# Performance work log

Hardware: AMD Instinct MI355X
Metric: run time of the kernel (lower is better)

Reference implementation:

```python
import jax, jax.numpy as jnp
import numpy as np

QMIN, QMAX = 0.0, 255.0  # uint8 affine quantization range


def setup_inputs() -> dict:
    key = jax.random.key(0)
    ks = jax.random.split(key, 7)
    B, S, IN, OUT = 4, 2048, 4096, 4096
    x = jax.random.normal(ks[0], (B, S, IN), dtype=jnp.float32)
    weight_q = jax.random.randint(ks[1], (OUT, IN), 0, 255, dtype=jnp.int32)
    weight_scales = jax.random.uniform(ks[2], (OUT,), dtype=jnp.float32) * 0.01 + 1e-4
    weight_zero_points = jax.random.randint(ks[3], (OUT,), 0, 255, dtype=jnp.int32)
    act_scales = jax.random.uniform(ks[4], (1,), dtype=jnp.float32) * 0.05 + 1e-3
    act_zero_points = jnp.full((1,), 128, dtype=jnp.int32)
    bias = jax.random.normal(ks[5], (OUT,), dtype=jnp.float32)
    return {
        "x": x,
        "weight_q": weight_q,
        "weight_scales": weight_scales,
        "weight_zero_points": weight_zero_points,
        "act_scales": act_scales,
        "act_zero_points": act_zero_points,
        "bias": bias,
    }


def reference(x, weight_q, weight_scales, weight_zero_points, act_scales, act_zero_points, bias):
    # quantize_from_qparams on activations (per-tensor affine, uint8 range)
    a_zp = act_zero_points.astype(jnp.float32)
    x_q = jnp.clip(jnp.round(x / act_scales) + a_zp, QMIN, QMAX)
    # linear_on_quantized_data: dequantize both operands, fused matmul + bias
    x_deq = (x_q - a_zp) * act_scales  # [B, S, IN]
    w_deq = (weight_q.astype(jnp.float32) - weight_zero_points.astype(jnp.float32)[:, None]) \
            * weight_scales[:, None]  # [OUT, IN], per-output-channel scale/zp
    out = jnp.einsum("bsi,oi->bso", x_deq, w_deq) + bias  # [B, S, OUT]
    return out
```

## Files before the change

### kernel.cpp

```cpp
#include <hip/hip_runtime.h>
#include <hip/hip_bf16.h>

using int32x4 = __attribute__((ext_vector_type(4))) int;

#define BM 256
#define BN 256
#define BKB 128

#define GATE(n) asm volatile("s_waitcnt vmcnt(" #n ")" ::: "memory")

__device__ __forceinline__ void load_lds16(const void* g, void* l) {
    __builtin_amdgcn_global_load_lds(
        (const __attribute__((address_space(1))) unsigned int*)g,
        (__attribute__((address_space(3))) unsigned int*)l, 16, 0, 0);
}

__global__ __launch_bounds__(256) void prep(
    const float* __restrict__ x, const float* __restrict__ act_scale,
    const int* __restrict__ act_zp, char* __restrict__ xs,
    int* __restrict__ rowsum, int K, int M,
    const int4* __restrict__ wq, char4* __restrict__ wsq, long n4)
{
    if (blockIdx.x < (unsigned)M) {
        __shared__ int wsum[4];
        const int row = blockIdx.x;
        const float s = act_scale[0];
        const int zp = act_zp[0];
        const float4* __restrict__ xr = (const float4*)(x + (size_t)row * K);
        char4* __restrict__ xo = (char4*)(xs + (size_t)row * K);
        const int nv = K >> 2;
        int sum = 0;
        for (int i = threadIdx.x; i < nv; i += 256) {
            float4 v = xr[i];
            int q0 = min(max((int)rintf(v.x / s) + zp, 0), 255) - zp;
            int q1 = min(max((int)rintf(v.y / s) + zp, 0), 255) - zp;
            int q2 = min(max((int)rintf(v.z / s) + zp, 0), 255) - zp;
            int q3 = min(max((int)rintf(v.w / s) + zp, 0), 255) - zp;
            sum += q0 + q1 + q2 + q3;
            char4 c;
            c.x = (char)q0; c.y = (char)q1; c.z = (char)q2; c.w = (char)q3;
            xo[i] = c;
        }
        for (int off = 32; off > 0; off >>= 1) sum += __shfl_down(sum, off, 64);
        if ((threadIdx.x & 63) == 0) wsum[threadIdx.x >> 6] = sum;
        __syncthreads();
        if (threadIdx.x == 0) rowsum[row] = wsum[0] + wsum[1] + wsum[2] + wsum[3];
    } else {
        long i = (long)(blockIdx.x - M) * 256 + threadIdx.x;
        if (i >= n4) return;
        int4 v = wq[i];
        char4 c;
        c.x = (char)(v.x - 128); c.y = (char)(v.y - 128);
        c.z = (char)(v.z - 128); c.w = (char)(v.w - 128);
        wsq[i] = c;
    }
}

__global__ __launch_bounds__(512, 2) void gemm_i8(
    const char* __restrict__ Aq, const char* __restrict__ Bq,
    const int* __restrict__ rowsum, const float* __restrict__ wscale,
    const int* __restrict__ wzp, const float* __restrict__ ascale,
    const float* __restrict__ bias, float* __restrict__ C,
    int M, int N, int K)
{
    __shared__ __align__(16) char As[2][BM * BKB];
    __shared__ __align__(16) char Bs[2][BN * BKB];

    const int tid = threadIdx.x;
    const int w   = tid >> 6;
    const int l   = tid & 63;

    const int nwg = gridDim.x;
    const int nbx = N / BN;
    const int orig = blockIdx.x;
    const int xcd = orig & 7;
    const int rest = orig >> 3;
    const int qq = nwg >> 3, rr = nwg & 7;
    const int wg = (xcd < rr ? xcd * (qq + 1) : rr * (qq + 1) + (xcd - rr) * qq)
                   + rest;
    const int n0 = (wg % nbx) * BN;
    const int m0 = (wg / nbx) * BM;

    const int wm = (w & 1) * 128;
    const int wn = (w >> 1) * 64;

    const int lr8 = l >> 3;
    const int csw = (((l & 7) ^ (lr8 & 7)) << 4);
    const int rB0 = w * 16;
    const int rA2 = (w < 4) ? (w * 16) : (128 + (w - 4) * 16);

    const char* sB0 = Bq + (size_t)(n0 + rB0 + lr8) * K + csw;
    const char* sB1 = sB0 + (size_t)128 * K;
    const char* sA2 = Aq + (size_t)(m0 + rA2 + lr8) * K + csw;
    const char* sA3 = sA2 + (size_t)64 * K;
    const size_t k8 = (size_t)8 * K;

    const int oB0 = rB0 * BKB;
    const int oB1 = oB0 + 128 * BKB;
    const int oA2 = rA2 * BKB;
    const int oA3 = oA2 + 64 * BKB;

    const int r   = l & 15;
    const int qk  = l >> 4;
    const int rx  = r & 7;
    const int rof = r * BKB;
    const int ck0 = ((qk ^ rx) << 4);
    const int ck1 = (((4 + qk) ^ rx) << 4);

    int32x4 acc[8][4] = {};
    const int NT = K / BKB;

    load_lds16(sB0,      Bs[0] + oB0);
    load_lds16(sB0 + k8, Bs[0] + oB0 + 1024);
    load_lds16(sB1,      Bs[0] + oB1);
    load_lds16(sB1 + k8, Bs[0] + oB1 + 1024);
    load_lds16(sA2,      As[0] + oA2);
    load_lds16(sA2 + k8, As[0] + oA2 + 1024);
    load_lds16(sA3,      As[0] + oA3);
    load_lds16(sA3 + k8, As[0] + oA3 + 1024);
    if (NT > 1) {
        load_lds16(sB0 + BKB,      Bs[1] + oB0);
        load_lds16(sB0 + BKB + k8, Bs[1] + oB0 + 1024);
        load_lds16(sB1 + BKB,      Bs[1] + oB1);
        load_lds16(sB1 + BKB + k8, Bs[1] + oB1 + 1024);
    }
    sA2 += BKB; sA3 += BKB;
    sB0 += 2 * (size_t)BKB; sB1 += 2 * (size_t)BKB;

    int s = 0;
    for (int T = 0; T < NT; ++T) {
        const char* cA = As[s];
        const char* cB = Bs[s];
        char* nA = As[s ^ 1];
        char* nB = Bs[s];
        const bool stA = (T + 1 < NT);
        const bool stB = (T + 2 < NT);
        int32x4 bf[4][2];
#pragma unroll
        for (int p = 0; p < 4; ++p) {
            if (p == 0) { if (stA) { GATE(6); } else { GATE(2); } }
            if (p == 2) { if (stA) { GATE(8); } else { GATE(0); } }
            __builtin_amdgcn_s_barrier();

            int32x4 af[2][2];
            const char* ab = cA + (wm + p * 32) * BKB + rof;
            af[0][0] = *(const int32x4*)(ab + ck0);
            af[0][1] = *(const int32x4*)(ab + ck1);
            af[1][0] = *(const int32x4*)(ab + 2048 + ck0);
            af[1][1] = *(const int32x4*)(ab + 2048 + ck1);
            if (p == 0) {
                const char* bb = cB + wn * BKB + rof;
#pragma unroll
                for (int j = 0; j < 4; ++j) {
                    bf[j][0] = *(const int32x4*)(bb + j * 2048 + ck0);
                    bf[j][1] = *(const int32x4*)(bb + j * 2048 + ck1);
                }
                if (stA) {
                    load_lds16(sA2,      nA + oA2);
                    load_lds16(sA2 + k8, nA + oA2 + 1024);
                    load_lds16(sA3,      nA + oA3);
                    load_lds16(sA3 + k8, nA + oA3 + 1024);
                }
            }
            if (p == 2 && stB) {
                load_lds16(sB0,      nB + oB0);
                load_lds16(sB0 + k8, nB + oB0 + 1024);
                load_lds16(sB1,      nB + oB1);
                load_lds16(sB1 + k8, nB + oB1 + 1024);
            }
            asm volatile("s_waitcnt lgkmcnt(0)" ::: "memory");
            __builtin_amdgcn_sched_barrier(0);
            __builtin_amdgcn_s_setprio(1);
#pragma unroll
            for (int i = 0; i < 2; ++i)
#pragma unroll
                for (int j = 0; j < 4; ++j) {
                    acc[p * 2 + i][j] = __builtin_amdgcn_mfma_i32_16x16x64_i8(
                        af[i][0], bf[j][0], acc[p * 2 + i][j], 0, 0, 0);
                    acc[p * 2 + i][j] = __builtin_amdgcn_mfma_i32_16x16x64_i8(
                        af[i][1], bf[j][1], acc[p * 2 + i][j], 0, 0, 0);
                }
            __builtin_amdgcn_s_setprio(0);
        }
        sA2 += BKB; sA3 += BKB; sB0 += BKB; sB1 += BKB;
        s ^= 1;
    }

    const float as = ascale[0];
    const int r4  = qk * 4;
    const int cil = r;
#pragma unroll
    for (int j = 0; j < 4; ++j) {
        const int col = n0 + wn + j * 16 + cil;
        const float al = as * wscale[col];
        const float be = al * (float)(128 - wzp[col]);
        const float bi = bias[col];
#pragma unroll
        for (int mi = 0; mi < 8; ++mi) {
            const int rowb = m0 + wm + mi * 16 + r4;
#pragma unroll
            for (int t = 0; t < 4; ++t) {
                const int row = rowb + t;
                C[(size_t)row * N + col] =
                    al * (float)acc[mi][j][t] + be * (float)rowsum[row] + bi;
            }
        }
    }
}

extern "C" void kernel_launch(void* const* d_in, const int* in_sizes, int n_in,
                              void* d_out, int out_size, void* d_ws, size_t ws_size,
                              hipStream_t stream) {
    const float* x      = (const float*)d_in[0];
    const int*   wq     = (const int*)d_in[1];
    const float* wscale = (const float*)d_in[2];
    const int*   wzp    = (const int*)d_in[3];
    const float* ascale = (const float*)d_in[4];
    const int*   azp    = (const int*)d_in[5];
    const float* bias   = (const float*)d_in[6];
    float* out = (float*)d_out;

    const int N = in_sizes[2];
    const int K = in_sizes[1] / N;
    const int M = in_sizes[0] / K;

    char* ws     = (char*)d_ws;
    char* xs     = ws;
    char* wsq    = ws + (size_t)M * K;
    int*  rowsum = (int*)(wsq + (size_t)N * K);

    long n4 = (long)N * K / 4;
    int wblocks = (int)((n4 + 255) / 256);
    prep<<<M + wblocks, 256, 0, stream>>>(
        x, ascale, azp, xs, rowsum, K, M, (const int4*)wq, (char4*)wsq, n4);

    dim3 grid((M / BM) * (N / BN));
    gemm_i8<<<grid, 512, 0, stream>>>(
        xs, wsq, rowsum, wscale, wzp, ascale, bias, out, M, N, K);
}
```

Baseline: 413.9 us.

## Restructure int8 GEMM main loop into ping-pong phases with split global loads

Rewrites the K-loop as four explicit phases, each issuing LDS fragment reads before a barrier and then an MFMA cluster. The A and B prefetches are split into pairs spread across the phases, and the vmcnt waits are moved so the next tile's data is gated at the end of each iteration instead of the start. The goal is a better spread of memory traffic and tighter overlap of LDS reads with MFMA work across waves. The cost is more barriers per iteration and wait counts that must stay consistent with the new load ordering.

```diff
diff --git a/kernel.cpp b/kernel.cpp
--- a/kernel.cpp
+++ b/kernel.cpp
@@ -8,6 +8,9 @@
 #define BKB 128
 
 #define GATE(n) asm volatile("s_waitcnt vmcnt(" #n ")" ::: "memory")
+#define LGKM(n) asm volatile("s_waitcnt lgkmcnt(" #n ")" ::: "memory")
+#define SCHED0() __builtin_amdgcn_sched_barrier(0)
+#define BAR() __builtin_amdgcn_s_barrier()
 
 __device__ __forceinline__ void load_lds16(const void* g, void* l) {
     __builtin_amdgcn_global_load_lds(
@@ -127,6 +130,31 @@
     sA2 += BKB; sA3 += BKB;
     sB0 += 2 * (size_t)BKB; sB1 += 2 * (size_t)BKB;
 
+    GATE(6);
+    BAR();
+
+#define READ_A(p)                                                       \
+    { const char* ab = cA + (wm + (p) * 32) * BKB + rof;                \
+      af[0][0] = *(const int32x4*)(ab + ck0);                           \
+      af[0][1] = *(const int32x4*)(ab + ck1);                           \
+      af[1][0] = *(const int32x4*)(ab + 2048 + ck0);                    \
+      af[1][1] = *(const int32x4*)(ab + 2048 + ck1); }
+
+#define CLUSTER(p)                                                      \
+    __builtin_amdgcn_s_setprio(1);                                      \
+    _Pragma("unroll")                                                   \
+    for (int i = 0; i < 2; ++i)                                         \
+        _Pragma("unroll")                                               \
+        for (int j = 0; j < 4; ++j) {                                   \
+            acc[(p)*2+i][j] = __builtin_amdgcn_mfma_i32_16x16x64_i8(    \
+                af[i][0], bf[j][0], acc[(p)*2+i][j], 0, 0, 0);          \
+            acc[(p)*2+i][j] = __builtin_amdgcn_mfma_i32_16x16x64_i8(    \
+                af[i][1], bf[j][1], acc[(p)*2+i][j], 0, 0, 0);          \
+        }                                                               \
+    __builtin_amdgcn_s_setprio(0);
+
+#define HEAD() SCHED0(); BAR(); LGKM(0); SCHED0()
+
     int s = 0;
     for (int T = 0; T < NT; ++T) {
         const char* cA = As[s];
@@ -135,53 +163,43 @@
         char* nB = Bs[s];
         const bool stA = (T + 1 < NT);
         const bool stB = (T + 2 < NT);
-        int32x4 bf[4][2];
-#pragma unroll
-        for (int p = 0; p < 4; ++p) {
-            if (p == 0) { if (stA) { GATE(6); } else { GATE(2); } }
-            if (p == 2) { if (stA) { GATE(8); } else { GATE(0); } }
-            __builtin_amdgcn_s_barrier();
-
-            int32x4 af[2][2];
-            const char* ab = cA + (wm + p * 32) * BKB + rof;
-            af[0][0] = *(const int32x4*)(ab + ck0);
-            af[0][1] = *(const int32x4*)(ab + ck1);
-            af[1][0] = *(const int32x4*)(ab + 2048 + ck0);
-            af[1][1] = *(const int32x4*)(ab + 2048 + ck1);
-            if (p == 0) {
-                const char* bb = cB + wn * BKB + rof;
-#pragma unroll
-                for (int j = 0; j < 4; ++j) {
-                    bf[j][0] = *(const int32x4*)(bb + j * 2048 + ck0);
-                    bf[j][1] = *(const int32x4*)(bb + j * 2048 + ck1);
-                }
-                if (stA) {
-                    load_lds16(sA2,      nA + oA2);
-                    load_lds16(sA2 + k8, nA + oA2 + 1024);
-                    load_lds16(sA3,      nA + oA3);
-                    load_lds16(sA3 + k8, nA + oA3 + 1024);
-                }
-            }
-            if (p == 2 && stB) {
-                load_lds16(sB0,      nB + oB0);
-                load_lds16(sB0 + k8, nB + oB0 + 1024);
-                load_lds16(sB1,      nB + oB1);
-                load_lds16(sB1 + k8, nB + oB1 + 1024);
-            }
-            asm volatile("s_waitcnt lgkmcnt(0)" ::: "memory");
-            __builtin_amdgcn_sched_barrier(0);
-            __builtin_amdgcn_s_setprio(1);
-#pragma unroll
-            for (int i = 0; i < 2; ++i)
-#pragma unroll
-                for (int j = 0; j < 4; ++j) {
-                    acc[p * 2 + i][j] = __builtin_amdgcn_mfma_i32_16x16x64_i8(
-                        af[i][0], bf[j][0], acc[p * 2 + i][j], 0, 0, 0);
-                    acc[p * 2 + i][j] = __builtin_amdgcn_mfma_i32_16x16x64_i8(
-                        af[i][1], bf[j][1], acc[p * 2 + i][j], 0, 0, 0);
-                }
-            __builtin_amdgcn_s_setprio(0);
-        }
+        int32x4 af[2][2], bf[4][2];
+
+        READ_A(0);
+        { const char* bb = cB + wn * BKB + rof;
+#pragma unroll
+          for (int j = 0; j < 4; ++j) {
+              bf[j][0] = *(const int32x4*)(bb + j * 2048 + ck0);
+              bf[j][1] = *(const int32x4*)(bb + j * 2048 + ck1);
+          } }
+        if (stA) { load_lds16(sA2,      nA + oA2);
+                   load_lds16(sA2 + k8, nA + oA2 + 1024); }
+        LGKM(8);
+        HEAD();
+        CLUSTER(0);
+        BAR();
+        READ_A(1);
+        if (stA) { load_lds16(sA3,      nA + oA3);
+                   load_lds16(sA3 + k8, nA + oA3 + 1024); }
+        HEAD();
+        CLUSTER(1);
+        if (stA) { GATE(8); } else { GATE(0); }
+        BAR();
+        READ_A(2);
+        if (stB) { load_lds16(sB0,      nB + oB0);
+                   load_lds16(sB0 + k8, nB + oB0 + 1024); }
+        HEAD();
+        CLUSTER(2);
+        BAR();
+        READ_A(3);
+        if (stB) { load_lds16(sB1,      nB + oB1);
+                   load_lds16(sB1 + k8, nB + oB1 + 1024); }
+        HEAD();
+        CLUSTER(3);
+        if (stB) { GATE(6); }
+        else if (stA) { GATE(2); }
+        BAR();
+
         sA2 += BKB; sA3 += BKB; sB0 += BKB; sB1 += BKB;
         s ^= 1;
     }
```

Result: slower. 434.6 us (+5.0%).
